# Kernel tuning notes

Hardware: AMD Instinct MI355X
Metric: run time of the kernel (lower is better)

## Reference

```python
import jax, jax.numpy as jnp
import numpy as np

N_STATE = 64   # n == m (required by the broadcast in the original forward)
SEQ_LEN = 200000


def setup_inputs() -> dict:
    key = jax.random.key(0)
    k_y, k_a, k_h = jax.random.split(key, 3)
    n = N_STATE
    # A scaled so spectral radius ~0.9 (stable recurrence), H ~ O(1) rows
    A = 0.9 * jax.random.normal(k_a, (n, n), dtype=jnp.float32) / jnp.sqrt(jnp.float32(n))
    H = jax.random.normal(k_h, (n, n), dtype=jnp.float32) / jnp.sqrt(jnp.float32(n))
    y = jax.random.normal(k_y, (n, SEQ_LEN), dtype=jnp.float32)
    L = jnp.float32(0.2)  # scalar learned gain (self.weights)
    return {"y": y, "A": A, "H": H, "L": L, "N": SEQ_LEN}


def reference(y, A, H, L, N):
    # x_{k+1} = A x_k + L * (y_k - H x_k);  yhat_k = H x_k  (pre-update state)
    # Vectorized over time with lax.scan (true sequential dependence).
    def step(x, yk):
        out = H @ x                      # [n] observation prediction at step k
        x_next = A @ x + L * (yk - out)  # [n] state update
        return x_next, out

    x0 = jnp.zeros((A.shape[0],), dtype=y.dtype)
    _, yhat_t = jax.lax.scan(step, x0, y.T)  # scan over time axis: y.T is [N, m]
    return yhat_t.T                          # [m, N]
```

## Files before the change

### kernel.cpp

```cpp
#include <hip/hip_runtime.h>


#define CHUNK 64
#define LOOKBACK 8

__device__ __forceinline__ float bcast(float x, int l) {
  return __uint_as_float(__builtin_amdgcn_readlane(__float_as_uint(x), l));
}

__global__ __launch_bounds__(1024) void kf_setup(const float* __restrict__ A,
                                                 const float* __restrict__ Hm,
                                                 const float* __restrict__ Lp,
                                                 float* __restrict__ ws) {
  __shared__ __align__(16) float s0[64 * 68];
  __shared__ __align__(16) float s1[64 * 68];
  const float Lg = Lp[0];
  const int t  = threadIdx.x;
  const int r  = t >> 4;
  const int c0 = (t & 15) * 4;

  if (t < 512) ws[4096 + t] = 0.f;

  {
    const float4 a4 = *(const float4*)(A  + r * 64 + c0);
    const float4 h4 = *(const float4*)(Hm + r * 64 + c0);
    float4 m4;
    m4.x = fmaf(-Lg, h4.x, a4.x);
    m4.y = fmaf(-Lg, h4.y, a4.y);
    m4.z = fmaf(-Lg, h4.z, a4.z);
    m4.w = fmaf(-Lg, h4.w, a4.w);
    *(float4*)(s0 + r * 68 + c0) = m4;
  }
  __syncthreads();

  float* src = s0;
  float* dst = s1;
  for (int sq = 0; sq < 6; ++sq) {
    float4 acc = make_float4(0.f, 0.f, 0.f, 0.f);
    const float* srow = src + r * 68;
    #pragma unroll 8
    for (int k = 0; k < 64; ++k) {
      const float  a  = srow[k];
      const float4 b4 = *(const float4*)(src + k * 68 + c0);
      acc.x = fmaf(a, b4.x, acc.x);
      acc.y = fmaf(a, b4.y, acc.y);
      acc.z = fmaf(a, b4.z, acc.z);
      acc.w = fmaf(a, b4.w, acc.w);
    }
    __syncthreads();
    *(float4*)(dst + r * 68 + c0) = acc;
    __syncthreads();
    float* tmp = src; src = dst; dst = tmp;
  }
  *(float4*)(ws + r * 64 + c0) = *(const float4*)(src + r * 68 + c0);
}

__global__ __launch_bounds__(64, 2) void kf_phase1(const float* __restrict__ y,
                                                   const float* __restrict__ A,
                                                   const float* __restrict__ Hm,
                                                   const float* __restrict__ Lp,
                                                   float* __restrict__ bb,
                                                   int Nv, int P) {
  const int lane = threadIdx.x;
  const float Lg = Lp[0];
  const int c0 = min(4 * (int)blockIdx.x + 0, P - 1);
  const int c1 = min(4 * (int)blockIdx.x + 1, P - 1);
  const int c2 = min(4 * (int)blockIdx.x + 2, P - 1);
  const int c3 = min(4 * (int)blockIdx.x + 3, P - 1);

  float Mrow[64];
  {
    const float* Ar = A  + lane * 64;
    const float* Hr = Hm + lane * 64;
    #pragma unroll
    for (int j = 0; j < 64; j += 4) {
      const float4 a4 = *(const float4*)(Ar + j);
      const float4 h4 = *(const float4*)(Hr + j);
      Mrow[j + 0] = fmaf(-Lg, h4.x, a4.x);
      Mrow[j + 1] = fmaf(-Lg, h4.y, a4.y);
      Mrow[j + 2] = fmaf(-Lg, h4.z, a4.z);
      Mrow[j + 3] = fmaf(-Lg, h4.w, a4.w);
    }
  }

  const float* yr0 = y + (size_t)lane * (size_t)Nv + c0 * CHUNK;
  const float* yr1 = y + (size_t)lane * (size_t)Nv + c1 * CHUNK;
  const float* yr2 = y + (size_t)lane * (size_t)Nv + c2 * CHUNK;
  const float* yr3 = y + (size_t)lane * (size_t)Nv + c3 * CHUNK;
  float x0 = 0.f, x1 = 0.f, x2 = 0.f, x3 = 0.f;

  #pragma unroll 1
  for (int t = 0; t < 8; ++t) {
    const float4 pa0 = *(const float4*)(yr0 + 8 * t);
    const float4 pb0 = *(const float4*)(yr0 + 8 * t + 4);
    const float4 pa1 = *(const float4*)(yr1 + 8 * t);
    const float4 pb1 = *(const float4*)(yr1 + 8 * t + 4);
    const float4 pa2 = *(const float4*)(yr2 + 8 * t);
    const float4 pb2 = *(const float4*)(yr2 + 8 * t + 4);
    const float4 pa3 = *(const float4*)(yr3 + 8 * t);
    const float4 pb3 = *(const float4*)(yr3 + 8 * t + 4);
    const float yb0[8] = {pa0.x, pa0.y, pa0.z, pa0.w, pb0.x, pb0.y, pb0.z, pb0.w};
    const float yb1[8] = {pa1.x, pa1.y, pa1.z, pa1.w, pb1.x, pb1.y, pb1.z, pb1.w};
    const float yb2[8] = {pa2.x, pa2.y, pa2.z, pa2.w, pb2.x, pb2.y, pb2.z, pb2.w};
    const float yb3[8] = {pa3.x, pa3.y, pa3.z, pa3.w, pb3.x, pb3.y, pb3.z, pb3.w};
    #pragma unroll
    for (int kk = 0; kk < 8; ++kk) {
      float a0 = 0.f, a1 = 0.f, a2 = 0.f, a3 = 0.f;
      #pragma unroll
      for (int j = 0; j < 64; ++j) {
        const float s0 = bcast(x0, j);
        const float s1 = bcast(x1, j);
        const float s2 = bcast(x2, j);
        const float s3 = bcast(x3, j);
        a0 = fmaf(Mrow[j], s0, a0);
        a1 = fmaf(Mrow[j], s1, a1);
        a2 = fmaf(Mrow[j], s2, a2);
        a3 = fmaf(Mrow[j], s3, a3);
      }
      x0 = fmaf(Lg, yb0[kk], a0);
      x1 = fmaf(Lg, yb1[kk], a1);
      x2 = fmaf(Lg, yb2[kk], a2);
      x3 = fmaf(Lg, yb3[kk], a3);
    }
  }
  bb[c0 * 64 + lane] = x0;
  bb[c1 * 64 + lane] = x1;
  bb[c2 * 64 + lane] = x2;
  bb[c3 * 64 + lane] = x3;
}

__global__ __launch_bounds__(64, 2) void kf_scan2(const float* __restrict__ y,
                                                  const float* __restrict__ A,
                                                  const float* __restrict__ Hm,
                                                  const float* __restrict__ Lp,
                                                  const float* __restrict__ bb,
                                                  const float* __restrict__ P64,
                                                  float* __restrict__ X,
                                                  int Nv, int P) {
  const int lane = threadIdx.x;
  const float Lg = Lp[0];
  const int c0 = min(2 * (int)blockIdx.x,     P - 1);
  const int c1 = min(2 * (int)blockIdx.x + 1, P - 1);

  float Mrow[64];
  {
    const float* Ar = A  + lane * 64;
    const float* Hr = Hm + lane * 64;
    #pragma unroll
    for (int j = 0; j < 64; j += 4) {
      const float4 a4 = *(const float4*)(Ar + j);
      const float4 h4 = *(const float4*)(Hr + j);
      Mrow[j + 0] = fmaf(-Lg, h4.x, a4.x);
      Mrow[j + 1] = fmaf(-Lg, h4.y, a4.y);
      Mrow[j + 2] = fmaf(-Lg, h4.z, a4.z);
      Mrow[j + 3] = fmaf(-Lg, h4.w, a4.w);
    }
  }

  float x0, x1;
  {
    float Prow[64];
    #pragma unroll
    for (int j = 0; j < 64; j += 4) {
      const float4 p4 = *(const float4*)(P64 + lane * 64 + j);
      Prow[j + 0] = p4.x; Prow[j + 1] = p4.y;
      Prow[j + 2] = p4.z; Prow[j + 3] = p4.w;
    }
    x0 = bb[(c0 - LOOKBACK) * 64 + lane];
    x1 = bb[(c1 - LOOKBACK) * 64 + lane];
    #pragma unroll 1
    for (int t = LOOKBACK - 1; t >= 1; --t) {
      float a0 = 0.f, a1 = 0.f, b0 = 0.f, b1 = 0.f;
      #pragma unroll
      for (int j = 0; j < 64; j += 2) {
        const float s0 = bcast(x0, j);
        const float s1 = bcast(x1, j);
        const float u0 = bcast(x0, j + 1);
        const float u1 = bcast(x1, j + 1);
        a0 = fmaf(Prow[j],     s0, a0);
        b0 = fmaf(Prow[j],     s1, b0);
        a1 = fmaf(Prow[j + 1], u0, a1);
        b1 = fmaf(Prow[j + 1], u1, b1);
      }
      x0 = (a0 + a1) + bb[(c0 - t) * 64 + lane];
      x1 = (b0 + b1) + bb[(c1 - t) * 64 + lane];
    }
  }

  const float* yr0 = y + (size_t)lane * (size_t)Nv + c0 * CHUNK;
  const float* yr1 = y + (size_t)lane * (size_t)Nv + c1 * CHUNK;
  float*       X0  = X + (size_t)lane * (size_t)Nv + c0 * CHUNK;
  float*       X1  = X + (size_t)lane * (size_t)Nv + c1 * CHUNK;

  #pragma unroll 1
  for (int t = 0; t < 8; ++t) {
    const float4 pa0 = *(const float4*)(yr0 + 8 * t);
    const float4 pb0 = *(const float4*)(yr0 + 8 * t + 4);
    const float4 pa1 = *(const float4*)(yr1 + 8 * t);
    const float4 pb1 = *(const float4*)(yr1 + 8 * t + 4);
    const float yb0[8] = {pa0.x, pa0.y, pa0.z, pa0.w, pb0.x, pb0.y, pb0.z, pb0.w};
    const float yb1[8] = {pa1.x, pa1.y, pa1.z, pa1.w, pb1.x, pb1.y, pb1.z, pb1.w};
    float xb0[8], xb1[8];

    #pragma unroll
    for (int kk = 0; kk < 8; ++kk) {
      xb0[kk] = x0;
      xb1[kk] = x1;
      float a0 = 0.f, a1 = 0.f, b0 = 0.f, b1 = 0.f;
      #pragma unroll
      for (int j = 0; j < 64; j += 2) {
        const float s0 = bcast(x0, j);
        const float s1 = bcast(x1, j);
        const float u0 = bcast(x0, j + 1);
        const float u1 = bcast(x1, j + 1);
        a0 = fmaf(Mrow[j],     s0, a0);
        b0 = fmaf(Mrow[j],     s1, b0);
        a1 = fmaf(Mrow[j + 1], u0, a1);
        b1 = fmaf(Mrow[j + 1], u1, b1);
      }
      x0 = fmaf(Lg, yb0[kk], a0 + a1);
      x1 = fmaf(Lg, yb1[kk], b0 + b1);
    }
    *(float4*)(X0 + 8 * t)     = make_float4(xb0[0], xb0[1], xb0[2], xb0[3]);
    *(float4*)(X0 + 8 * t + 4) = make_float4(xb0[4], xb0[5], xb0[6], xb0[7]);
    *(float4*)(X1 + 8 * t)     = make_float4(xb1[0], xb1[1], xb1[2], xb1[3]);
    *(float4*)(X1 + 8 * t + 4) = make_float4(xb1[4], xb1[5], xb1[6], xb1[7]);
  }
}

__global__ __launch_bounds__(64, 4) void kf_hgemm(const float* __restrict__ Hm,
                                                  float* xo, int Nv) {
  const int lane = threadIdx.x;
  const int k    = (int)blockIdx.x * CHUNK + lane;

  float xcol[64];
  #pragma unroll
  for (int r = 0; r < 64; ++r) {
    xcol[r] = xo[(size_t)r * (size_t)Nv + k];
  }

  #pragma unroll 1
  for (int r = 0; r < 64; ++r) {
    const float* hr = Hm + r * 64;
    float a0 = 0.f, a1 = 0.f;
    #pragma unroll
    for (int j = 0; j < 64; j += 2) {
      a0 = fmaf(hr[j],     xcol[j],     a0);
      a1 = fmaf(hr[j + 1], xcol[j + 1], a1);
    }
    xo[(size_t)r * (size_t)Nv + k] = a0 + a1;
  }
}

extern "C" void kernel_launch(void* const* d_in, const int* in_sizes, int n_in,
                              void* d_out, int out_size, void* d_ws, size_t ws_size,
                              hipStream_t stream) {
  const float* y  = (const float*)d_in[0];
  const float* A  = (const float*)d_in[1];
  const float* Hm = (const float*)d_in[2];
  const float* Lp = (const float*)d_in[3];
  const int Nv = in_sizes[0] / 64;
  const int P  = (Nv + CHUNK - 1) / CHUNK;

  float* ws   = (float*)d_ws;
  float* P64  = ws;
  float* bb   = ws + 4096 + 512;

  kf_setup<<<1, 1024, 0, stream>>>(A, Hm, Lp, ws);
  kf_phase1<<<(P + 3) / 4, 64, 0, stream>>>(y, A, Hm, Lp, bb, Nv, P);
  kf_scan2<<<(P + 1) / 2, 64, 0, stream>>>(y, A, Hm, Lp, bb, P64, (float*)d_out, Nv, P);
  kf_hgemm<<<P, 64, 0, stream>>>(Hm, (float*)d_out, Nv);
}
```

Baseline: 279.9 us.

## Replace two-pass chunk scan with local scan plus matrix-power correction pass

Drops the separate phase-1 pass that computed chunk-end states. Each chunk is now scanned from a zero state, writing local states and chunk ends in one pass. A second kernel combines the lookback carries and builds the carry's propagation through powers of M by repeated doubling with the stored M^(2^t) matrices. It adds that correction to the local states before the H projection. This removes one full sequential recurrence over y, at the cost of extra correction work per chunk and an extra read-modify of the state buffer.

```diff
diff --git a/kernel.cpp b/kernel.cpp
--- a/kernel.cpp
+++ b/kernel.cpp
@@ -19,7 +19,7 @@
   const int r  = t >> 4;
   const int c0 = (t & 15) * 4;
 
-  if (t < 512) ws[4096 + t] = 0.f;
+  if (t < 512) ws[7 * 4096 + t] = 0.f;
 
   {
     const float4 a4 = *(const float4*)(A  + r * 64 + c0);
@@ -36,6 +36,7 @@
   float* src = s0;
   float* dst = s1;
   for (int sq = 0; sq < 6; ++sq) {
+    *(float4*)(ws + sq * 4096 + r * 64 + c0) = *(const float4*)(src + r * 68 + c0);
     float4 acc = make_float4(0.f, 0.f, 0.f, 0.f);
     const float* srow = src + r * 68;
     #pragma unroll 8
@@ -52,21 +53,20 @@
     __syncthreads();
     float* tmp = src; src = dst; dst = tmp;
   }
-  *(float4*)(ws + r * 64 + c0) = *(const float4*)(src + r * 68 + c0);
-}
-
-__global__ __launch_bounds__(64, 2) void kf_phase1(const float* __restrict__ y,
-                                                   const float* __restrict__ A,
-                                                   const float* __restrict__ Hm,
-                                                   const float* __restrict__ Lp,
-                                                   float* __restrict__ bb,
-                                                   int Nv, int P) {
+  *(float4*)(ws + 6 * 4096 + r * 64 + c0) = *(const float4*)(src + r * 68 + c0);
+}
+
+__global__ __launch_bounds__(64, 2) void kf_scan(const float* __restrict__ y,
+                                                 const float* __restrict__ A,
+                                                 const float* __restrict__ Hm,
+                                                 const float* __restrict__ Lp,
+                                                 float* __restrict__ bb,
+                                                 float* __restrict__ X,
+                                                 int Nv, int P) {
   const int lane = threadIdx.x;
   const float Lg = Lp[0];
-  const int c0 = min(4 * (int)blockIdx.x + 0, P - 1);
-  const int c1 = min(4 * (int)blockIdx.x + 1, P - 1);
-  const int c2 = min(4 * (int)blockIdx.x + 2, P - 1);
-  const int c3 = min(4 * (int)blockIdx.x + 3, P - 1);
+  const int c0 = min(2 * (int)blockIdx.x,     P - 1);
+  const int c1 = min(2 * (int)blockIdx.x + 1, P - 1);
 
   float Mrow[64];
   {
@@ -85,112 +85,9 @@
 
   const float* yr0 = y + (size_t)lane * (size_t)Nv + c0 * CHUNK;
   const float* yr1 = y + (size_t)lane * (size_t)Nv + c1 * CHUNK;
-  const float* yr2 = y + (size_t)lane * (size_t)Nv + c2 * CHUNK;
-  const float* yr3 = y + (size_t)lane * (size_t)Nv + c3 * CHUNK;
-  float x0 = 0.f, x1 = 0.f, x2 = 0.f, x3 = 0.f;
-
-  #pragma unroll 1
-  for (int t = 0; t < 8; ++t) {
-    const float4 pa0 = *(const float4*)(yr0 + 8 * t);
-    const float4 pb0 = *(const float4*)(yr0 + 8 * t + 4);
-    const float4 pa1 = *(const float4*)(yr1 + 8 * t);
-    const float4 pb1 = *(const float4*)(yr1 + 8 * t + 4);
-    const float4 pa2 = *(const float4*)(yr2 + 8 * t);
-    const float4 pb2 = *(const float4*)(yr2 + 8 * t + 4);
-    const float4 pa3 = *(const float4*)(yr3 + 8 * t);
-    const float4 pb3 = *(const float4*)(yr3 + 8 * t + 4);
-    const float yb0[8] = {pa0.x, pa0.y, pa0.z, pa0.w, pb0.x, pb0.y, pb0.z, pb0.w};
-    const float yb1[8] = {pa1.x, pa1.y, pa1.z, pa1.w, pb1.x, pb1.y, pb1.z, pb1.w};
-    const float yb2[8] = {pa2.x, pa2.y, pa2.z, pa2.w, pb2.x, pb2.y, pb2.z, pb2.w};
-    const float yb3[8] = {pa3.x, pa3.y, pa3.z, pa3.w, pb3.x, pb3.y, pb3.z, pb3.w};
-    #pragma unroll
-    for (int kk = 0; kk < 8; ++kk) {
-      float a0 = 0.f, a1 = 0.f, a2 = 0.f, a3 = 0.f;
-      #pragma unroll
-      for (int j = 0; j < 64; ++j) {
-        const float s0 = bcast(x0, j);
-        const float s1 = bcast(x1, j);
-        const float s2 = bcast(x2, j);
-        const float s3 = bcast(x3, j);
-        a0 = fmaf(Mrow[j], s0, a0);
-        a1 = fmaf(Mrow[j], s1, a1);
-        a2 = fmaf(Mrow[j], s2, a2);
-        a3 = fmaf(Mrow[j], s3, a3);
-      }
-      x0 = fmaf(Lg, yb0[kk], a0);
-      x1 = fmaf(Lg, yb1[kk], a1);
-      x2 = fmaf(Lg, yb2[kk], a2);
-      x3 = fmaf(Lg, yb3[kk], a3);
-    }
-  }
-  bb[c0 * 64 + lane] = x0;
-  bb[c1 * 64 + lane] = x1;
-  bb[c2 * 64 + lane] = x2;
-  bb[c3 * 64 + lane] = x3;
-}
-
-__global__ __launch_bounds__(64, 2) void kf_scan2(const float* __restrict__ y,
-                                                  const float* __restrict__ A,
-                                                  const float* __restrict__ Hm,
-                                                  const float* __restrict__ Lp,
-                                                  const float* __restrict__ bb,
-                                                  const float* __restrict__ P64,
-                                                  float* __restrict__ X,
-                                                  int Nv, int P) {
-  const int lane = threadIdx.x;
-  const float Lg = Lp[0];
-  const int c0 = min(2 * (int)blockIdx.x,     P - 1);
-  const int c1 = min(2 * (int)blockIdx.x + 1, P - 1);
-
-  float Mrow[64];
-  {
-    const float* Ar = A  + lane * 64;
-    const float* Hr = Hm + lane * 64;
-    #pragma unroll
-    for (int j = 0; j < 64; j += 4) {
-      const float4 a4 = *(const float4*)(Ar + j);
-      const float4 h4 = *(const float4*)(Hr + j);
-      Mrow[j + 0] = fmaf(-Lg, h4.x, a4.x);
-      Mrow[j + 1] = fmaf(-Lg, h4.y, a4.y);
-      Mrow[j + 2] = fmaf(-Lg, h4.z, a4.z);
-      Mrow[j + 3] = fmaf(-Lg, h4.w, a4.w);
-    }
-  }
-
-  float x0, x1;
-  {
-    float Prow[64];
-    #pragma unroll
-    for (int j = 0; j < 64; j += 4) {
-      const float4 p4 = *(const float4*)(P64 + lane * 64 + j);
-      Prow[j + 0] = p4.x; Prow[j + 1] = p4.y;
-      Prow[j + 2] = p4.z; Prow[j + 3] = p4.w;
-    }
-    x0 = bb[(c0 - LOOKBACK) * 64 + lane];
-    x1 = bb[(c1 - LOOKBACK) * 64 + lane];
-    #pragma unroll 1
-    for (int t = LOOKBACK - 1; t >= 1; --t) {
-      float a0 = 0.f, a1 = 0.f, b0 = 0.f, b1 = 0.f;
-      #pragma unroll
-      for (int j = 0; j < 64; j += 2) {
-        const float s0 = bcast(x0, j);
-        const float s1 = bcast(x1, j);
-        const float u0 = bcast(x0, j + 1);
-        const float u1 = bcast(x1, j + 1);
-        a0 = fmaf(Prow[j],     s0, a0);
-        b0 = fmaf(Prow[j],     s1, b0);
-        a1 = fmaf(Prow[j + 1], u0, a1);
-        b1 = fmaf(Prow[j + 1], u1, b1);
-      }
-      x0 = (a0 + a1) + bb[(c0 - t) * 64 + lane];
-      x1 = (b0 + b1) + bb[(c1 - t) * 64 + lane];
-    }
-  }
-
-  const float* yr0 = y + (size_t)lane * (size_t)Nv + c0 * CHUNK;
-  const float* yr1 = y + (size_t)lane * (size_t)Nv + c1 * CHUNK;
   float*       X0  = X + (size_t)lane * (size_t)Nv + c0 * CHUNK;
   float*       X1  = X + (size_t)lane * (size_t)Nv + c1 * CHUNK;
+  float x0 = 0.f, x1 = 0.f;
 
   #pragma unroll 1
   for (int t = 0; t < 8; ++t) {
@@ -226,29 +123,105 @@
     *(float4*)(X1 + 8 * t)     = make_float4(xb1[0], xb1[1], xb1[2], xb1[3]);
     *(float4*)(X1 + 8 * t + 4) = make_float4(xb1[4], xb1[5], xb1[6], xb1[7]);
   }
-}
-
-__global__ __launch_bounds__(64, 4) void kf_hgemm(const float* __restrict__ Hm,
-                                                  float* xo, int Nv) {
+  bb[c0 * 64 + lane] = x0;
+  bb[c1 * 64 + lane] = x1;
+}
+
+__global__ __launch_bounds__(64, 2) void kf_zh(const float* __restrict__ Hm,
+                                               const float* __restrict__ ws,
+                                               const float* __restrict__ bb,
+                                               float* xo, int Nv) {
   const int lane = threadIdx.x;
-  const int k    = (int)blockIdx.x * CHUNK + lane;
-
-  float xcol[64];
-  #pragma unroll
-  for (int r = 0; r < 64; ++r) {
-    xcol[r] = xo[(size_t)r * (size_t)Nv + k];
-  }
-
+  const int c    = (int)blockIdx.x;
+  __shared__ __align__(16) float z[64][68];
+
+  float s;
+  {
+    float Prow[64];
+    #pragma unroll
+    for (int j = 0; j < 64; j += 4) {
+      const float4 p4 = *(const float4*)(ws + 6 * 4096 + lane * 64 + j);
+      Prow[j + 0] = p4.x; Prow[j + 1] = p4.y;
+      Prow[j + 2] = p4.z; Prow[j + 3] = p4.w;
+    }
+    s = bb[(c - LOOKBACK) * 64 + lane];
+    #pragma unroll 1
+    for (int t = LOOKBACK - 1; t >= 1; --t) {
+      float a0 = 0.f, a1 = 0.f;
+      #pragma unroll
+      for (int j = 0; j < 64; j += 2) {
+        a0 = fmaf(Prow[j],     bcast(s, j),     a0);
+        a1 = fmaf(Prow[j + 1], bcast(s, j + 1), a1);
+      }
+      s = (a0 + a1) + bb[(c - t) * 64 + lane];
+    }
+  }
+
+  z[lane][0] = s;
+  __syncthreads();
+
+  #pragma unroll 1
+  for (int t = 0; t < 6; ++t) {
+    float Mp[64];
+    #pragma unroll
+    for (int j = 0; j < 64; j += 4) {
+      const float4 m4 = *(const float4*)(ws + t * 4096 + lane * 64 + j);
+      Mp[j + 0] = m4.x; Mp[j + 1] = m4.y;
+      Mp[j + 2] = m4.z; Mp[j + 3] = m4.w;
+    }
+    const int w = 1 << t;
+    if (w < 4) {
+      #pragma unroll
+      for (int k = 0; k < 2; ++k) {
+        if (k < w) {
+          float a0 = 0.f, a1 = 0.f;
+          #pragma unroll
+          for (int j = 0; j < 64; j += 2) {
+            a0 = fmaf(Mp[j],     z[j][k],     a0);
+            a1 = fmaf(Mp[j + 1], z[j + 1][k], a1);
+          }
+          z[lane][k + w] = a0 + a1;
+        }
+      }
+    } else {
+      #pragma unroll 1
+      for (int k = 0; k < w; k += 4) {
+        float a0 = 0.f, a1 = 0.f, a2 = 0.f, a3 = 0.f;
+        #pragma unroll
+        for (int j = 0; j < 64; ++j) {
+          const float4 zv = *(const float4*)&z[j][k];
+          const float  m  = Mp[j];
+          a0 = fmaf(m, zv.x, a0);
+          a1 = fmaf(m, zv.y, a1);
+          a2 = fmaf(m, zv.z, a2);
+          a3 = fmaf(m, zv.w, a3);
+        }
+        *(float4*)&z[lane][k + w] = make_float4(a0, a1, a2, a3);
+      }
+    }
+    __syncthreads();
+  }
+
+  float zcol[64];
+  {
+    const float* xc = xo + (size_t)c * CHUNK + lane;
+    #pragma unroll 8
+    for (int j = 0; j < 64; ++j) {
+      zcol[j] = z[j][lane] + xc[(size_t)j * (size_t)Nv];
+    }
+  }
+
+  float* oc = xo + (size_t)c * CHUNK + lane;
   #pragma unroll 1
   for (int r = 0; r < 64; ++r) {
     const float* hr = Hm + r * 64;
     float a0 = 0.f, a1 = 0.f;
     #pragma unroll
     for (int j = 0; j < 64; j += 2) {
-      a0 = fmaf(hr[j],     xcol[j],     a0);
-      a1 = fmaf(hr[j + 1], xcol[j + 1], a1);
-    }
-    xo[(size_t)r * (size_t)Nv + k] = a0 + a1;
+      a0 = fmaf(hr[j],     zcol[j],     a0);
+      a1 = fmaf(hr[j + 1], zcol[j + 1], a1);
+    }
+    oc[(size_t)r * (size_t)Nv] = a0 + a1;
   }
 }
 
@@ -262,12 +235,10 @@
   const int Nv = in_sizes[0] / 64;
   const int P  = (Nv + CHUNK - 1) / CHUNK;
 
-  float* ws   = (float*)d_ws;
-  float* P64  = ws;
-  float* bb   = ws + 4096 + 512;
+  float* ws = (float*)d_ws;
+  float* bb = ws + 7 * 4096 + 512;
 
   kf_setup<<<1, 1024, 0, stream>>>(A, Hm, Lp, ws);
-  kf_phase1<<<(P + 3) / 4, 64, 0, stream>>>(y, A, Hm, Lp, bb, Nv, P);
-  kf_scan2<<<(P + 1) / 2, 64, 0, stream>>>(y, A, Hm, Lp, bb, P64, (float*)d_out, Nv, P);
-  kf_hgemm<<<P, 64, 0, stream>>>(Hm, (float*)d_out, Nv);
-}
+  kf_scan<<<(P + 1) / 2, 64, 0, stream>>>(y, A, Hm, Lp, bb, (float*)d_out, Nv, P);
+  kf_zh<<<P, 64, 0, stream>>>(Hm, ws, bb, (float*)d_out, Nv);
+}
```

Result: no change. 279.6 us (-0.1%).
